# Kernel optimization log

Hardware: AMD Instinct MI355X
Metric: run time of the kernel (lower is better)

## Reference

```python
import jax, jax.numpy as jnp
import numpy as np
from jax import lax

WIN_SIZE = 11
SIGMA = 1.5
K1, K2 = 0.01, 0.03
DATA_RANGE = 1.0


def _gaussian_window():
    coords = jnp.arange(WIN_SIZE, dtype=jnp.float32) - (WIN_SIZE - 1) / 2.0
    g = jnp.exp(-(coords ** 2) / (2.0 * SIGMA ** 2))
    return g / jnp.sum(g)


def _gaussian_filter(x, win):
    # x: (B, C, H, W); separable depthwise gaussian blur, VALID padding
    C = x.shape[1]
    dn = ('NCHW', 'OIHW', 'NCHW')
    kh = jnp.broadcast_to(win.reshape(1, 1, WIN_SIZE, 1), (C, 1, WIN_SIZE, 1))
    kw = jnp.broadcast_to(win.reshape(1, 1, 1, WIN_SIZE), (C, 1, 1, WIN_SIZE))
    x = lax.conv_general_dilated(x, kh, (1, 1), 'VALID', dimension_numbers=dn, feature_group_count=C)
    x = lax.conv_general_dilated(x, kw, (1, 1), 'VALID', dimension_numbers=dn, feature_group_count=C)
    return x


def _ssim_per_image(X, Y):
    # X, Y: (B, C, H, W) -> (B,) SSIM averaged over channels and spatial (pytorch_msssim, size_average=False)
    win = _gaussian_window()
    C1 = (K1 * DATA_RANGE) ** 2
    C2 = (K2 * DATA_RANGE) ** 2
    mu1 = _gaussian_filter(X, win)
    mu2 = _gaussian_filter(Y, win)
    mu1_sq = mu1 * mu1
    mu2_sq = mu2 * mu2
    mu1_mu2 = mu1 * mu2
    sigma1_sq = _gaussian_filter(X * X, win) - mu1_sq
    sigma2_sq = _gaussian_filter(Y * Y, win) - mu2_sq
    sigma12 = _gaussian_filter(X * Y, win) - mu1_mu2
    ssim_map = ((2.0 * mu1_mu2 + C1) * (2.0 * sigma12 + C2)) / (
        (mu1_sq + mu2_sq + C1) * (sigma1_sq + sigma2_sq + C2))
    return jnp.mean(ssim_map, axis=(1, 2, 3))


def setup_inputs() -> dict:
    key = jax.random.key(0)
    k1, k2 = jax.random.split(key)
    x1 = jax.random.normal(k1, (15, 441, 64), dtype=jnp.float32)
    x2 = jax.random.normal(k2, (5, 5, 441, 64), dtype=jnp.float32)
    return {"x1": x1, "x2": x2}


def reference(x1, x2):
    B, h, w, C = 15, 21, 21, 64
    N, S = x2.shape[0], x2.shape[1]
    # queries: view(15,21,21,64).permute(0,3,1,2) -> (15,64,21,21)
    q = jnp.transpose(x1.reshape(B, h, w, C), (0, 3, 1, 2))
    # per-(h,w) L2 normalization over channel dim (dim 0 of each sample)
    q = q / jnp.linalg.norm(q, axis=1, keepdims=True)
    # supports: (N,5,441,64).permute(0,1,3,2).view -> (N,5,64,21,21)
    s = jnp.transpose(x2, (0, 1, 3, 2)).reshape(N, S, C, h, w)
    s = s / jnp.linalg.norm(s, axis=2, keepdims=True)
    # pairwise broadcast: every query against every support image of every class
    Xb = jnp.broadcast_to(q[:, None, None], (B, N, S, C, h, w)).reshape(B * N * S, C, h, w)
    Yb = jnp.broadcast_to(s[None], (B, N, S, C, h, w)).reshape(B * N * S, C, h, w)
    sims = _ssim_per_image(Xb, Yb).reshape(B, N, S)
    # inner_sim[0, j] = sum of SSIM over the S shots
    return jnp.sum(sims, axis=2)  # (15, N)
```

## Files before the change

kernel.cpp:

```cpp
#include <hip/hip_runtime.h>

#define BQ   15
#define NIMG 40
#define CH   64
#define HW   21
#define P    441
#define WIN  11
#define OH   11
#define OP   121
#define TP   231

#define P1_UNITS 840
#define P2_UNITS 1280
#define P3_UNITS 6000

__device__ __forceinline__ float Wf(int a) {
    constexpr float w[WIN] = {
        0.0010283804f, 0.0075988025f, 0.0360007770f, 0.1093606993f,
        0.2130055427f, 0.2660117290f, 0.2130055427f, 0.1093606993f,
        0.0360007770f, 0.0075988025f, 0.0010283804f};
    return w[a];
}

__global__ void __launch_bounds__(256) k_prep(const float* __restrict__ x1,
                                              const float* __restrict__ x2,
                                              float* __restrict__ tn,
                                              float* __restrict__ out) {
    __shared__ float lds[1432];
    const int tid = threadIdx.x;
    if (blockIdx.x == 0 && tid < BQ * 5) out[tid] = 0.f;

    int u = blockIdx.x;
    int img = u / 21, chunk = u - img * 21;
    int p0 = chunk * 21;
    const float* src = (img < BQ) ? (x1 + (size_t)img * P * CH)
                                  : (x2 + (size_t)(img - BQ) * P * CH);
    src += (size_t)p0 * CH;
    float* dst = tn + (size_t)img * CH * P;
    float* invn = lds + 1408;

    const float4* src4 = reinterpret_cast<const float4*>(src);
    for (int i4 = tid; i4 < 21 * CH / 4; i4 += 256) {
        float4 v = src4[i4];
        int e = i4 * 4, p = e >> 6, c = e & 63;
        float* d = &lds[p * 65 + c];
        d[0] = v.x; d[1] = v.y; d[2] = v.z; d[3] = v.w;
    }
    __syncthreads();
    if (tid < 84) {
        int p = tid >> 2, q = tid & 3;
        const float* row = lds + p * 65 + q * 16;
        float s = 0.f;
#pragma unroll
        for (int c = 0; c < 16; ++c) s = fmaf(row[c], row[c], s);
        s += __shfl_xor(s, 1, 64);
        s += __shfl_xor(s, 2, 64);
        if (q == 0) invn[p] = rsqrtf(s);
    }
    __syncthreads();
    for (int i = tid; i < 21 * CH; i += 256) {
        int c = i / 21, p = i - c * 21;
        dst[(size_t)c * P + p0 + p] = lds[p * 65 + c] * invn[p];
    }
}

__global__ void __launch_bounds__(256) k_stats(const float* __restrict__ tn,
                                               float* __restrict__ mu,
                                               float* __restrict__ sq) {
    __shared__ float lds[1824];
    const int tid = threadIdx.x;
    int u = blockIdx.x;
    int img = u >> 5, cp = u & 31;
    const float* src = tn + ((size_t)img * CH + cp * 2) * P;

    for (int i = tid; i < 2 * P; i += 256) {
        int k = i / P, t = i - k * P;
        lds[k * 448 + t] = src[i];
    }
    __syncthreads();
    for (int i = tid; i < 2 * TP; i += 256) {
        int k = i / TP, t = i - k * TP;
        const float* x = lds + k * 448;
        float a1 = 0.f, a2 = 0.f;
#pragma unroll
        for (int a = 0; a < WIN; ++a) {
            float v = x[t + 21 * a];
            a1 = fmaf(Wf(a), v, a1);
            a2 = fmaf(Wf(a) * v, v, a2);
        }
        lds[896 + k * 232 + t]  = a1;
        lds[1360 + k * 232 + t] = a2;
    }
    __syncthreads();
    for (int i = tid; i < 2 * OP; i += 256) {
        int k = i / OP, t = i - k * OP;
        int r = t / OH, cc = t - r * OH;
        int b0 = r * HW + cc;
        const float* t1 = lds + 896 + k * 232;
        const float* t2 = lds + 1360 + k * 232;
        float a1 = 0.f, a2 = 0.f;
#pragma unroll
        for (int a = 0; a < WIN; ++a) {
            a1 = fmaf(Wf(a), t1[b0 + a], a1);
            a2 = fmaf(Wf(a), t2[b0 + a], a2);
        }
        size_t o = ((size_t)img * CH + cp * 2) * OP + i;
        mu[o] = a1;
        sq[o] = a2;
    }
}

__global__ void __launch_bounds__(256) k_pairs(const float* __restrict__ tn,
                                               const float* __restrict__ mu,
                                               const float* __restrict__ sq,
                                               float* __restrict__ out) {
    __shared__ float lds[2720];
    __shared__ float ws4[4];
    const float C1 = 1e-4f, C2 = 9e-4f;
    const int tid = threadIdx.x;

    int u = blockIdx.x;
    int chunk = u / 375, pair = u - chunk * 375;
    int b = pair / 25, rem = pair - b * 25;
    int ch0 = chunk * 4;
    const float* X = tn + ((size_t)b * CH + ch0) * P;
    const float* Y = tn + ((size_t)(BQ + rem) * CH + ch0) * P;
    size_t oq = ((size_t)b * CH + ch0) * OP;
    size_t os = ((size_t)(BQ + rem) * CH + ch0) * OP;

    float m1r[2], m2r[2], s1r[2], s2r[2];
#pragma unroll
    for (int j = 0; j < 2; ++j) {
        int i3 = tid + j * 256;
        int ii = (i3 < 4 * OP) ? i3 : 0;
        m1r[j] = mu[oq + ii]; m2r[j] = mu[os + ii];
        s1r[j] = sq[oq + ii]; s2r[j] = sq[os + ii];
    }

    const float4* X4 = reinterpret_cast<const float4*>(X);
    const float4* Y4 = reinterpret_cast<const float4*>(Y);
    for (int i4 = tid; i4 < 4 * P / 4; i4 += 256) {
        float4 xv = X4[i4], yv = Y4[i4];
        int e = i4 * 4;
#pragma unroll
        for (int j = 0; j < 4; ++j) {
            int ee = e + j;
            int k = ee / P, t = ee - k * P;
            lds[k * 448 + t] = (&xv.x)[j] * (&yv.x)[j];
        }
    }
    __syncthreads();
    for (int i = tid; i < 4 * TP; i += 256) {
        int k = i / TP, t = i - k * TP;
        const float* x = lds + k * 448;
        float a1 = 0.f;
#pragma unroll
        for (int a = 0; a < WIN; ++a) a1 = fmaf(Wf(a), x[t + 21 * a], a1);
        lds[1792 + k * 232 + t] = a1;
    }
    __syncthreads();

    float part = 0.f;
#pragma unroll
    for (int j = 0; j < 2; ++j) {
        int i3 = tid + j * 256;
        if (i3 < 4 * OP) {
            int k = i3 / OP, t = i3 - k * OP;
            int r = t / OH, cc = t - r * OH;
            const float* t1 = lds + 1792 + k * 232;
            float sxy = 0.f;
#pragma unroll
            for (int a = 0; a < WIN; ++a) sxy = fmaf(Wf(a), t1[r * HW + cc + a], sxy);
            float m1 = m1r[j], m2 = m2r[j];
            float v1 = s1r[j] - m1 * m1;
            float v2 = s2r[j] - m2 * m2;
            float cov = sxy - m1 * m2;
            part += ((2.f * m1 * m2 + C1) * (2.f * cov + C2)) /
                    ((m1 * m1 + m2 * m2 + C1) * (v1 + v2 + C2));
        }
    }
#pragma unroll
    for (int off = 32; off > 0; off >>= 1) part += __shfl_down(part, off, 64);
    if ((tid & 63) == 0) ws4[tid >> 6] = part;
    __syncthreads();
    if (tid == 0) {
        int n = rem / 5;
        atomicAdd(&out[b * 5 + n],
                  (ws4[0] + ws4[1] + ws4[2] + ws4[3]) * (1.0f / (CH * OP)));
    }
}

extern "C" void kernel_launch(void* const* d_in, const int* in_sizes, int n_in,
                              void* d_out, int out_size, void* d_ws, size_t ws_size,
                              hipStream_t stream) {
    const float* x1 = (const float*)d_in[0];
    const float* x2 = (const float*)d_in[1];
    float* out = (float*)d_out;
    float* ws  = (float*)d_ws;

    float* tn = ws;
    float* mu = tn + (size_t)NIMG * CH * P;
    float* sq = mu + (size_t)NIMG * CH * OP;

    k_prep <<<P1_UNITS, 256, 0, stream>>>(x1, x2, tn, out);
    k_stats<<<P2_UNITS, 256, 0, stream>>>(tn, mu, sq);
    k_pairs<<<P3_UNITS, 256, 0, stream>>>(tn, mu, sq, out);
}
```

Baseline: 101.7 us.

## Fuse normalization and per-image blur stats into one kernel; widen pair blocks to 8 channels

Merges the normalize/transpose kernel with the mu/sq blur-statistics kernel, so each block loads a whole image, computes the channel L2 norms with wave shuffles, keeps a 16-channel transposed tile in LDS, writes tn, and computes the stats from LDS. This removes one launch and a round trip of tn through global memory. Each block recomputes the norms from all 64 channels, and only 160 blocks run this stage. The pairs kernel now handles 8 channels per block on a 2D grid (3000 blocks instead of 6000), which amortizes per-block overhead but raises LDS and register use per block.

```diff
diff --git a/kernel.cpp b/kernel.cpp
--- a/kernel.cpp
+++ b/kernel.cpp
@@ -10,10 +10,6 @@
 #define OP   121
 #define TP   231
 
-#define P1_UNITS 840
-#define P2_UNITS 1280
-#define P3_UNITS 6000
-
 __device__ __forceinline__ float Wf(int a) {
     constexpr float w[WIN] = {
         0.0010283804f, 0.0075988025f, 0.0360007770f, 0.1093606993f,
@@ -22,91 +18,82 @@
     return w[a];
 }
 
-__global__ void __launch_bounds__(256) k_prep(const float* __restrict__ x1,
-                                              const float* __restrict__ x2,
-                                              float* __restrict__ tn,
-                                              float* __restrict__ out) {
-    __shared__ float lds[1432];
+__global__ void __launch_bounds__(256) k_ps(const float* __restrict__ x1,
+                                            const float* __restrict__ x2,
+                                            float* __restrict__ tn,
+                                            float* __restrict__ mu,
+                                            float* __restrict__ sq,
+                                            float* __restrict__ out) {
+    __shared__ float tile[16 * 449];
+    __shared__ float t1[8 * 232];
+    __shared__ float t2[8 * 232];
     const int tid = threadIdx.x;
     if (blockIdx.x == 0 && tid < BQ * 5) out[tid] = 0.f;
 
-    int u = blockIdx.x;
-    int img = u / 21, chunk = u - img * 21;
-    int p0 = chunk * 21;
+    const int img = blockIdx.x >> 2, cg = blockIdx.x & 3;
     const float* src = (img < BQ) ? (x1 + (size_t)img * P * CH)
                                   : (x2 + (size_t)(img - BQ) * P * CH);
-    src += (size_t)p0 * CH;
-    float* dst = tn + (size_t)img * CH * P;
-    float* invn = lds + 1408;
+    const int wv = tid >> 6, grp = (tid & 63) >> 4, sub = tid & 15;
 
-    const float4* src4 = reinterpret_cast<const float4*>(src);
-    for (int i4 = tid; i4 < 21 * CH / 4; i4 += 256) {
-        float4 v = src4[i4];
-        int e = i4 * 4, p = e >> 6, c = e & 63;
-        float* d = &lds[p * 65 + c];
-        d[0] = v.x; d[1] = v.y; d[2] = v.z; d[3] = v.w;
+#pragma unroll 4
+    for (int it = 0; it < 28; ++it) {
+        int p = it * 16 + wv * 4 + grp;
+        float4 v = make_float4(0.f, 0.f, 0.f, 0.f);
+        if (p < P) v = *reinterpret_cast<const float4*>(src + (size_t)p * CH + sub * 4);
+        float s = fmaf(v.x, v.x, fmaf(v.y, v.y, fmaf(v.z, v.z, v.w * v.w)));
+        s += __shfl_xor(s, 1, 64);
+        s += __shfl_xor(s, 2, 64);
+        s += __shfl_xor(s, 4, 64);
+        s += __shfl_xor(s, 8, 64);
+        int c0 = sub * 4 - cg * 16;
+        if (p < P && c0 >= 0 && c0 < 16) {
+            float inv = rsqrtf(s);
+            tile[(c0 + 0) * 449 + p] = v.x * inv;
+            tile[(c0 + 1) * 449 + p] = v.y * inv;
+            tile[(c0 + 2) * 449 + p] = v.z * inv;
+            tile[(c0 + 3) * 449 + p] = v.w * inv;
+        }
     }
     __syncthreads();
-    if (tid < 84) {
-        int p = tid >> 2, q = tid & 3;
-        const float* row = lds + p * 65 + q * 16;
-        float s = 0.f;
+
+    {
+        float* dst = tn + ((size_t)img * CH + cg * 16) * P;
+        for (int i = tid; i < 16 * P; i += 256) {
+            int c = i / P, p = i - c * P;
+            dst[i] = tile[c * 449 + p];
+        }
+    }
+
+    for (int pass = 0; pass < 2; ++pass) {
+        if (pass) __syncthreads();
+        for (int i = tid; i < 8 * TP; i += 256) {
+            int k = i / TP, t = i - k * TP;
+            const float* x = tile + (pass * 8 + k) * 449;
+            float a1 = 0.f, a2 = 0.f;
 #pragma unroll
-        for (int c = 0; c < 16; ++c) s = fmaf(row[c], row[c], s);
-        s += __shfl_xor(s, 1, 64);
-        s += __shfl_xor(s, 2, 64);
-        if (q == 0) invn[p] = rsqrtf(s);
-    }
-    __syncthreads();
-    for (int i = tid; i < 21 * CH; i += 256) {
-        int c = i / 21, p = i - c * 21;
-        dst[(size_t)c * P + p0 + p] = lds[p * 65 + c] * invn[p];
-    }
-}
-
-__global__ void __launch_bounds__(256) k_stats(const float* __restrict__ tn,
-                                               float* __restrict__ mu,
-                                               float* __restrict__ sq) {
-    __shared__ float lds[1824];
-    const int tid = threadIdx.x;
-    int u = blockIdx.x;
-    int img = u >> 5, cp = u & 31;
-    const float* src = tn + ((size_t)img * CH + cp * 2) * P;
-
-    for (int i = tid; i < 2 * P; i += 256) {
-        int k = i / P, t = i - k * P;
-        lds[k * 448 + t] = src[i];
-    }
-    __syncthreads();
-    for (int i = tid; i < 2 * TP; i += 256) {
-        int k = i / TP, t = i - k * TP;
-        const float* x = lds + k * 448;
-        float a1 = 0.f, a2 = 0.f;
+            for (int a = 0; a < WIN; ++a) {
+                float v = x[t + 21 * a];
+                a1 = fmaf(Wf(a), v, a1);
+                a2 = fmaf(Wf(a) * v, v, a2);
+            }
+            t1[k * 232 + t] = a1;
+            t2[k * 232 + t] = a2;
+        }
+        __syncthreads();
+        for (int i = tid; i < 8 * OP; i += 256) {
+            int k = i / OP, t = i - k * OP;
+            int r = t / OH, cc = t - r * OH;
+            int b0 = r * HW + cc;
+            float a1 = 0.f, a2 = 0.f;
 #pragma unroll
-        for (int a = 0; a < WIN; ++a) {
-            float v = x[t + 21 * a];
-            a1 = fmaf(Wf(a), v, a1);
-            a2 = fmaf(Wf(a) * v, v, a2);
+            for (int a = 0; a < WIN; ++a) {
+                a1 = fmaf(Wf(a), t1[k * 232 + b0 + a], a1);
+                a2 = fmaf(Wf(a), t2[k * 232 + b0 + a], a2);
+            }
+            size_t o = ((size_t)img * CH + cg * 16 + pass * 8 + k) * OP + t;
+            mu[o] = a1;
+            sq[o] = a2;
         }
-        lds[896 + k * 232 + t]  = a1;
-        lds[1360 + k * 232 + t] = a2;
-    }
-    __syncthreads();
-    for (int i = tid; i < 2 * OP; i += 256) {
-        int k = i / OP, t = i - k * OP;
-        int r = t / OH, cc = t - r * OH;
-        int b0 = r * HW + cc;
-        const float* t1 = lds + 896 + k * 232;
-        const float* t2 = lds + 1360 + k * 232;
-        float a1 = 0.f, a2 = 0.f;
-#pragma unroll
-        for (int a = 0; a < WIN; ++a) {
-            a1 = fmaf(Wf(a), t1[b0 + a], a1);
-            a2 = fmaf(Wf(a), t2[b0 + a], a2);
-        }
-        size_t o = ((size_t)img * CH + cp * 2) * OP + i;
-        mu[o] = a1;
-        sq[o] = a2;
     }
 }
 
@@ -114,63 +101,62 @@
                                                const float* __restrict__ mu,
                                                const float* __restrict__ sq,
                                                float* __restrict__ out) {
-    __shared__ float lds[2720];
+    __shared__ float xy[8 * 448];
+    __shared__ float tb[8 * 232];
     __shared__ float ws4[4];
     const float C1 = 1e-4f, C2 = 9e-4f;
     const int tid = threadIdx.x;
 
-    int u = blockIdx.x;
-    int chunk = u / 375, pair = u - chunk * 375;
+    int pair = blockIdx.x;
     int b = pair / 25, rem = pair - b * 25;
-    int ch0 = chunk * 4;
-    const float* X = tn + ((size_t)b * CH + ch0) * P;
-    const float* Y = tn + ((size_t)(BQ + rem) * CH + ch0) * P;
-    size_t oq = ((size_t)b * CH + ch0) * OP;
-    size_t os = ((size_t)(BQ + rem) * CH + ch0) * OP;
+    int cb = blockIdx.y * 8;
+    const float* X = tn + ((size_t)b * CH + cb) * P;
+    const float* Y = tn + ((size_t)(BQ + rem) * CH + cb) * P;
+    size_t oq = ((size_t)b * CH + cb) * OP;
+    size_t os = ((size_t)(BQ + rem) * CH + cb) * OP;
 
-    float m1r[2], m2r[2], s1r[2], s2r[2];
+    float m1r[4], m2r[4], s1r[4], s2r[4];
 #pragma unroll
-    for (int j = 0; j < 2; ++j) {
+    for (int j = 0; j < 4; ++j) {
         int i3 = tid + j * 256;
-        int ii = (i3 < 4 * OP) ? i3 : 0;
+        int ii = (i3 < 8 * OP) ? i3 : 0;
         m1r[j] = mu[oq + ii]; m2r[j] = mu[os + ii];
         s1r[j] = sq[oq + ii]; s2r[j] = sq[os + ii];
     }
 
     const float4* X4 = reinterpret_cast<const float4*>(X);
     const float4* Y4 = reinterpret_cast<const float4*>(Y);
-    for (int i4 = tid; i4 < 4 * P / 4; i4 += 256) {
+    for (int i4 = tid; i4 < 8 * P / 4; i4 += 256) {
         float4 xv = X4[i4], yv = Y4[i4];
         int e = i4 * 4;
 #pragma unroll
         for (int j = 0; j < 4; ++j) {
             int ee = e + j;
             int k = ee / P, t = ee - k * P;
-            lds[k * 448 + t] = (&xv.x)[j] * (&yv.x)[j];
+            xy[k * 448 + t] = (&xv.x)[j] * (&yv.x)[j];
         }
     }
     __syncthreads();
-    for (int i = tid; i < 4 * TP; i += 256) {
+    for (int i = tid; i < 8 * TP; i += 256) {
         int k = i / TP, t = i - k * TP;
-        const float* x = lds + k * 448;
+        const float* x = xy + k * 448;
         float a1 = 0.f;
 #pragma unroll
         for (int a = 0; a < WIN; ++a) a1 = fmaf(Wf(a), x[t + 21 * a], a1);
-        lds[1792 + k * 232 + t] = a1;
+        tb[k * 232 + t] = a1;
     }
     __syncthreads();
 
     float part = 0.f;
 #pragma unroll
-    for (int j = 0; j < 2; ++j) {
+    for (int j = 0; j < 4; ++j) {
         int i3 = tid + j * 256;
-        if (i3 < 4 * OP) {
+        if (i3 < 8 * OP) {
             int k = i3 / OP, t = i3 - k * OP;
             int r = t / OH, cc = t - r * OH;
-            const float* t1 = lds + 1792 + k * 232;
             float sxy = 0.f;
 #pragma unroll
-            for (int a = 0; a < WIN; ++a) sxy = fmaf(Wf(a), t1[r * HW + cc + a], sxy);
+            for (int a = 0; a < WIN; ++a) sxy = fmaf(Wf(a), tb[k * 232 + r * HW + cc + a], sxy);
             float m1 = m1r[j], m2 = m2r[j];
             float v1 = s1r[j] - m1 * m1;
             float v2 = s2r[j] - m2 * m2;
@@ -202,7 +188,6 @@
     float* mu = tn + (size_t)NIMG * CH * P;
     float* sq = mu + (size_t)NIMG * CH * OP;
 
-    k_prep <<<P1_UNITS, 256, 0, stream>>>(x1, x2, tn, out);
-    k_stats<<<P2_UNITS, 256, 0, stream>>>(tn, mu, sq);
-    k_pairs<<<P3_UNITS, 256, 0, stream>>>(tn, mu, sq, out);
+    k_ps   <<<NIMG * 4, 256, 0, stream>>>(x1, x2, tn, mu, sq, out);
+    k_pairs<<<dim3(375, 8), 256, 0, stream>>>(tn, mu, sq, out);
 }
```

Measured after the change: 104.6 us. 2.9% more time.
